# Performance work log

Measured on AMD Instinct MI355X. Metric: run time of the kernel, lower is better.

The kernel has to match this reference:

```python
import jax, jax.numpy as jnp
import numpy as np

HEADS = 2

def gat_layer(x, edge_index, W, att, bias):
    # x: [N, Fin], W: [H*C, Fin], att: [1, H, 2C], bias: [C]
    N = x.shape[0]
    C = bias.shape[0]
    # add self loops (source_to_target: x_j from row 0, aggregate onto row 1)
    loop = jnp.arange(N, dtype=edge_index.dtype)
    src = jnp.concatenate([edge_index[0], loop])
    dst = jnp.concatenate([edge_index[1], loop])
    h = (x @ W.T).reshape(N, HEADS, C)          # [N, H, C]
    x_j = h[src]                                 # [E, H, C]
    x_i = h[dst]                                 # [E, H, C]
    x_cat = jnp.concatenate([x_i, x_j], axis=-1) # [E, H, 2C]
    alpha = (x_cat * att).sum(-1)                # [E, H]
    alpha = jnp.where(alpha >= 0, alpha, 0.2 * alpha)  # leaky_relu(0.2)
    # NOTE: module uses a global (not per-destination) normalization
    alpha = jnp.exp(alpha - alpha.max())
    alpha = alpha / (alpha.sum(axis=0, keepdims=True) + 1e-10)
    msg = x_j * alpha[..., None]                 # [E, H, C]
    aggr = jax.ops.segment_sum(msg, dst, num_segments=N)  # [N, H, C]
    return aggr.mean(axis=1) + bias              # [N, C]

def setup_inputs() -> dict:
    key = jax.random.key(0)
    ks = jax.random.split(key, 7)
    N, Fin, C = 50000, 128, 64
    E = 800000
    x = jax.random.normal(ks[0], (N, Fin), dtype=jnp.float32)
    edge_index = jax.random.randint(ks[1], (2, E), 0, N, dtype=jnp.int64)
    W1 = jax.random.normal(ks[2], (HEADS * C, Fin), dtype=jnp.float32) * 0.05
    att1 = jax.random.normal(ks[3], (1, HEADS, 2 * C), dtype=jnp.float32) * 0.05
    b1 = jnp.zeros((C,), dtype=jnp.float32)
    W2 = jax.random.normal(ks[4], (HEADS * C, C), dtype=jnp.float32) * 0.05
    att2 = jax.random.normal(ks[5], (1, HEADS, 2 * C), dtype=jnp.float32) * 0.05
    b2 = jnp.zeros((C,), dtype=jnp.float32)
    return {"x": x, "edge_index": edge_index, "W1": W1, "att1": att1,
            "b1": b1, "W2": W2, "att2": att2, "b2": b2}

def reference(x, edge_index, W1, att1, b1, W2, att2, b2):
    h = gat_layer(x, edge_index, W1, att1, b1)
    h = jax.nn.relu(h)
    # F.dropout with training flag: treated as eval (identity) for determinism
    out = gat_layer(h, edge_index, W2, att2, b2)
    return out
```

## Files before the change

kernel.cpp:

```cpp
#include <hip/hip_runtime.h>
#include <hip/hip_bf16.h>
#include <math.h>


#define HP 8
#define HG 64
#define NHISTB (HP * HG)
#define HRANGE_MAX 6272
#define NZ    256

using short8 = __attribute__((ext_vector_type(8))) short;
using f32x4  = __attribute__((ext_vector_type(4))) float;

__device__ __forceinline__ unsigned f2bf(float x) {
  unsigned u = __float_as_uint(x);
  return (u + 0x7fffu + ((u >> 16) & 1u)) >> 16;
}
__device__ __forceinline__ float bflo(unsigned p) { return __uint_as_float(p << 16); }
__device__ __forceinline__ float bfhi(unsigned p) { return __uint_as_float(p & 0xffff0000u); }

__global__ __launch_bounds__(256) void init_ws(
    const float* __restrict__ W1, const float* __restrict__ W2,
    unsigned short* __restrict__ wbf1, unsigned short* __restrict__ wbf2,
    float* __restrict__ Z) {
  int tid = blockIdx.x * 256 + threadIdx.x;
  int stride = gridDim.x * 256;
  for (int i = tid; i < 128 * 128; i += stride)
    wbf1[i] = (unsigned short)f2bf(W1[i]);
  for (int i = tid; i < 128 * 64; i += stride)
    wbf2[i] = (unsigned short)f2bf(W2[i]);
  if (tid < 4) Z[tid] = 0.f;
}

template <int FIN>
__global__ __launch_bounds__(256) void gemm_mfma(
    const float* __restrict__ x, const unsigned short* __restrict__ Wb,
    const float* __restrict__ att, unsigned* __restrict__ hq,
    float* __restrict__ si, float* __restrict__ sj,
    int N,
    const int* __restrict__ dstE, int* __restrict__ partial,
    int E, int nhistb, int hstep) {
  const int tid = threadIdx.x;

  constexpr int WB = 128 * FIN * 2;
  constexpr int SMEM = (WB > HRANGE_MAX * 4) ? WB : HRANGE_MAX * 4;
  __shared__ __align__(16) unsigned char smem[SMEM];

  if ((int)blockIdx.x < nhistb) {
    int* lhist = (int*)smem;
    const int p = blockIdx.x & (HP - 1);
    const int g = blockIdx.x >> 3;
    const int lo = p * hstep;
    for (int i = tid; i < hstep; i += 256) lhist[i] = 0;
    __syncthreads();
    const int stride = HG * 256;
    int e = g * 256 + tid;
    for (; e + 3 * stride < E; e += 4 * stride) {
      int d0 = dstE[e] - lo;
      int d1 = dstE[e + stride] - lo;
      int d2 = dstE[e + 2 * stride] - lo;
      int d3 = dstE[e + 3 * stride] - lo;
      if ((unsigned)d0 < (unsigned)hstep) atomicAdd(&lhist[d0], 1);
      if ((unsigned)d1 < (unsigned)hstep) atomicAdd(&lhist[d1], 1);
      if ((unsigned)d2 < (unsigned)hstep) atomicAdd(&lhist[d2], 1);
      if ((unsigned)d3 < (unsigned)hstep) atomicAdd(&lhist[d3], 1);
    }
    for (; e < E; e += stride) {
      int d = dstE[e] - lo;
      if ((unsigned)d < (unsigned)hstep) atomicAdd(&lhist[d], 1);
    }
    __syncthreads();
    for (int i = tid; i < hstep; i += 256) {
      int node = lo + i;
      if (node < N) partial[(size_t)g * N + node] = lhist[i];
    }
    return;
  }

  constexpr int KS = FIN / 32;
  constexpr int CPR = FIN / 8;
  constexpr int NCHUNK = 128 * CPR;

  unsigned short* wlds = (unsigned short*)smem;

  const int w    = tid >> 6;
  const int lane = tid & 63;
  const int cl   = lane & 15;
  const int grp  = lane >> 4;
  const int n0   = (blockIdx.x - nhistb) * 64;

  const int arow = n0 + w * 16 + cl;
  const bool avalid = arow < N;
  float4 av0[KS], av1[KS];
#pragma unroll
  for (int ks = 0; ks < KS; ++ks) {
    av0[ks] = make_float4(0.f, 0.f, 0.f, 0.f);
    av1[ks] = av0[ks];
    if (avalid) {
      const float4* xp =
          (const float4*)(x + (size_t)arow * FIN + ks * 32 + grp * 8);
      av0[ks] = xp[0];
      av1[ks] = xp[1];
    }
  }

  const uint4* Wb4 = (const uint4*)Wb;
  for (int c = tid; c < NCHUNK; c += 256) {
    int row = c / CPR;
    int cc  = c & (CPR - 1);
    *(uint4*)&wlds[row * FIN + ((cc ^ (row & (CPR - 1))) * 8)] = Wb4[c];
  }
  __syncthreads();

  short8 afrag[KS];
#pragma unroll
  for (int ks = 0; ks < KS; ++ks) {
    union { short8 s8; unsigned u[4]; } af;
    af.u[0] = f2bf(av0[ks].x) | (f2bf(av0[ks].y) << 16);
    af.u[1] = f2bf(av0[ks].z) | (f2bf(av0[ks].w) << 16);
    af.u[2] = f2bf(av1[ks].x) | (f2bf(av1[ks].y) << 16);
    af.u[3] = f2bf(av1[ks].z) | (f2bf(av1[ks].w) << 16);
    afrag[ks] = af.s8;
  }

  f32x4 acc[8];
#pragma unroll
  for (int ct = 0; ct < 8; ++ct) acc[ct] = (f32x4){0.f, 0.f, 0.f, 0.f};

  const int swz = cl & (CPR - 1);
#pragma unroll
  for (int ks = 0; ks < KS; ++ks) {
#pragma unroll
    for (int ct = 0; ct < 8; ++ct) {
      const unsigned short* bp =
          &wlds[(ct * 16 + cl) * FIN + (((ks * 4 + grp) ^ swz) * 8)];
      short8 bfrag = *(const short8*)bp;
      acc[ct] = __builtin_amdgcn_mfma_f32_16x16x32_bf16(afrag[ks], bfrag,
                                                        acc[ct], 0, 0, 0);
    }
  }

  float ai[8], aj[8];
#pragma unroll
  for (int ct = 0; ct < 8; ++ct) {
    int hd = ct >> 2;
    int cw = (ct & 3) * 16 + cl;
    ai[ct] = att[hd * 128 + cw];
    aj[ct] = att[hd * 128 + 64 + cw];
  }

#pragma unroll
  for (int r = 0; r < 4; ++r) {
    int node = n0 + w * 16 + grp * 4 + r;
    float s0i = 0.f, s0j = 0.f, s1i = 0.f, s1j = 0.f;
    unsigned wpk[4];
#pragma unroll
    for (int ct = 0; ct < 4; ++ct) {
      float v0 = acc[ct][r];
      float v1 = acc[ct + 4][r];
      s0i += v0 * ai[ct];
      s0j += v0 * aj[ct];
      s1i += v1 * ai[ct + 4];
      s1j += v1 * aj[ct + 4];
      wpk[ct] = f2bf(v0) | (f2bf(v1) << 16);
    }
#pragma unroll
    for (int off = 8; off; off >>= 1) {
      s0i += __shfl_xor(s0i, off, 64);
      s0j += __shfl_xor(s0j, off, 64);
      s1i += __shfl_xor(s1i, off, 64);
      s1j += __shfl_xor(s1j, off, 64);
    }
    if (node < N) {
#pragma unroll
      for (int ct = 0; ct < 4; ++ct)
        hq[(size_t)node * 64 + ct * 16 + cl] = wpk[ct];
      if (cl == 0) {
        si[node * 2 + 0] = s0i;
        si[node * 2 + 1] = s1i;
        sj[node * 2 + 0] = s0j;
        sj[node * 2 + 1] = s1j;
      }
    }
  }
}

__global__ __launch_bounds__(256) void reduce_deg(
    const int* __restrict__ partial, int* __restrict__ deg, int N) {
  int i = blockIdx.x * 256 + threadIdx.x;
  int stride = gridDim.x * 256;
  for (; i < N; i += stride) {
    int s = 0;
#pragma unroll
    for (int g = 0; g < HG; ++g) s += partial[(size_t)g * N + i];
    deg[i] = s;
  }
}

__device__ __forceinline__ void z_edge_body(
    const int* __restrict__ srcE, const int* __restrict__ dstE,
    const float2* __restrict__ si2, const float2* __restrict__ sj2,
    float* __restrict__ Zp, int E, int Etot, int tid0, int stride) {
  float z0 = 0.f, z1 = 0.f;
  for (int e = tid0; e < Etot; e += stride) {
    int s, d;
    if (e < E) { s = srcE[e]; d = dstE[e]; } else { s = d = e - E; }
    float2 siv = si2[d];
    float2 sjv = sj2[s];
    float a0 = siv.x + sjv.x;
    float a1 = siv.y + sjv.y;
    a0 = a0 >= 0.f ? a0 : 0.2f * a0;
    a1 = a1 >= 0.f ? a1 : 0.2f * a1;
    z0 += __expf(a0); z1 += __expf(a1);
  }
  __shared__ float r0[4], r1[4];
  int lane = threadIdx.x & 63, w = threadIdx.x >> 6;
#pragma unroll
  for (int off = 32; off; off >>= 1) {
    z0 += __shfl_down(z0, off, 64);
    z1 += __shfl_down(z1, off, 64);
  }
  if (lane == 0) { r0[w] = z0; r1[w] = z1; }
  __syncthreads();
  if (threadIdx.x == 0) {
    atomicAdd(&Zp[0], r0[0] + r0[1] + r0[2] + r0[3]);
    atomicAdd(&Zp[1], r1[0] + r1[1] + r1[2] + r1[3]);
  }
}

__global__ __launch_bounds__(256) void z_edge(
    const int* __restrict__ srcE, const int* __restrict__ dstE,
    const float2* __restrict__ si2, const float2* __restrict__ sj2,
    float* __restrict__ Zp, int E, int Etot) {
  z_edge_body(srcE, dstE, si2, sj2, Zp, E, Etot,
              blockIdx.x * 256 + threadIdx.x, gridDim.x * 256);
}

__global__ __launch_bounds__(256) void scan_blocks(
    const int* __restrict__ deg, int* __restrict__ rowptr,
    int* __restrict__ bsum, int N) {
  __shared__ int ts[256];
  int b = blockIdx.x, t = threadIdx.x;
  int base = b * 1024 + t * 4;
  int v[4];
#pragma unroll
  for (int j = 0; j < 4; ++j) v[j] = (base + j < N) ? deg[base + j] : 0;
  int tot = v[0] + v[1] + v[2] + v[3];
  ts[t] = tot;
  __syncthreads();
#pragma unroll
  for (int off = 1; off < 256; off <<= 1) {
    int x = (t >= off) ? ts[t - off] : 0;
    __syncthreads();
    ts[t] += x;
    __syncthreads();
  }
  int run = ts[t] - tot;
#pragma unroll
  for (int j = 0; j < 4; ++j) {
    if (base + j < N) rowptr[base + j] = run;
    run += v[j];
  }
  if (t == 255) bsum[b] = ts[255];
}

__global__ __launch_bounds__(256) void scan_finish(
    int* __restrict__ rowptr, const int* __restrict__ bsum,
    int* __restrict__ partial, int N, int Eall, int nb) {
  __shared__ int pre[256];
  if (threadIdx.x == 0) {
    int run = 0;
    for (int i = 0; i < nb; ++i) { pre[i] = run; run += bsum[i]; }
  }
  __syncthreads();
  int tid = blockIdx.x * blockDim.x + threadIdx.x;
  int stride = gridDim.x * blockDim.x;
  for (int i = tid; i < N; i += stride) {
    int v = rowptr[i] + pre[i >> 10];
    rowptr[i] = v;
    int run = v;
#pragma unroll 8
    for (int g = 0; g < HG; ++g) {
      int c = partial[(size_t)g * N + i];
      partial[(size_t)g * N + i] = run;
      run += c;
    }
  }
  if (tid == 0) rowptr[N] = Eall;
}

__global__ __launch_bounds__(256) void scatter_z(
    const int* __restrict__ srcE, const int* __restrict__ dstE,
    const int* __restrict__ partial, int* __restrict__ esrc,
    const float2* __restrict__ si2, const float2* __restrict__ sj2,
    float* __restrict__ Zp, int E, int Etot, int hstep, int N) {
  __shared__ __align__(16) int lcur[HRANGE_MAX];
  if ((int)blockIdx.x < NZ) {
    z_edge_body(srcE, dstE, si2, sj2, Zp, E, Etot,
                blockIdx.x * 256 + threadIdx.x, NZ * 256);
    return;
  }
  const int bid = blockIdx.x - NZ;
  const int p = bid & (HP - 1);
  const int g = bid >> 3;
  const int lo = p * hstep;
  const int tid = threadIdx.x;
  for (int i = tid; i < hstep; i += 256) {
    int node = lo + i;
    lcur[i] = (node < N) ? partial[(size_t)g * N + node] : 0;
  }
  __syncthreads();
  const int stride = HG * 256;
  int e = g * 256 + tid;
  for (; e + 3 * stride < E; e += 4 * stride) {
    int d0 = dstE[e] - lo;
    int d1 = dstE[e + stride] - lo;
    int d2 = dstE[e + 2 * stride] - lo;
    int d3 = dstE[e + 3 * stride] - lo;
    if ((unsigned)d0 < (unsigned)hstep) esrc[atomicAdd(&lcur[d0], 1)] = srcE[e];
    if ((unsigned)d1 < (unsigned)hstep) esrc[atomicAdd(&lcur[d1], 1)] = srcE[e + stride];
    if ((unsigned)d2 < (unsigned)hstep) esrc[atomicAdd(&lcur[d2], 1)] = srcE[e + 2 * stride];
    if ((unsigned)d3 < (unsigned)hstep) esrc[atomicAdd(&lcur[d3], 1)] = srcE[e + 3 * stride];
  }
  for (; e < E; e += stride) {
    int d = dstE[e] - lo;
    if ((unsigned)d < (unsigned)hstep) esrc[atomicAdd(&lcur[d], 1)] = srcE[e];
  }
}

__global__ __launch_bounds__(256) void csr_aggregate(
    const int* __restrict__ rowptr, const int* __restrict__ esrc,
    const unsigned* __restrict__ hq, const float2* __restrict__ si2,
    const float2* __restrict__ sj2, const float* __restrict__ Zp,
    const float* __restrict__ bias, float* __restrict__ out,
    int N, int do_relu) {
  int lane = threadIdx.x & 63;
  int wid = (blockIdx.x * blockDim.x + threadIdx.x) >> 6;
  int nw = (gridDim.x * blockDim.x) >> 6;
  float z0 = 1.f / (Zp[0] + 1e-10f);
  float z1 = 1.f / (Zp[1] + 1e-10f);
  float bv = bias[lane];
  for (int n0 = wid; n0 < N; n0 += nw) {
    int n = __builtin_amdgcn_readfirstlane(n0);
    int beg = rowptr[n], end = rowptr[n + 1];
    float2 siv = si2[n];
    float acc0, acc1;
    {
      float2 jv = sj2[n];
      unsigned p = hq[(size_t)n * 64 + lane];
      float a0 = siv.x + jv.x, a1 = siv.y + jv.y;
      a0 = a0 >= 0.f ? a0 : 0.2f * a0;
      a1 = a1 >= 0.f ? a1 : 0.2f * a1;
      acc0 = bflo(p) * __expf(a0);
      acc1 = bfhi(p) * __expf(a1);
    }
    int k = beg;
    for (; k + 4 <= end; k += 4) {
      int s0 = esrc[k], s1 = esrc[k + 1], s2 = esrc[k + 2], s3 = esrc[k + 3];
      float2 j0 = sj2[s0], j1 = sj2[s1], j2 = sj2[s2], j3 = sj2[s3];
      unsigned p0 = hq[(size_t)s0 * 64 + lane];
      unsigned p1 = hq[(size_t)s1 * 64 + lane];
      unsigned p2 = hq[(size_t)s2 * 64 + lane];
      unsigned p3 = hq[(size_t)s3 * 64 + lane];
      float a00 = siv.x + j0.x, a01 = siv.y + j0.y;
      float a10 = siv.x + j1.x, a11 = siv.y + j1.y;
      float a20 = siv.x + j2.x, a21 = siv.y + j2.y;
      float a30 = siv.x + j3.x, a31 = siv.y + j3.y;
      a00 = a00 >= 0.f ? a00 : 0.2f * a00;  a01 = a01 >= 0.f ? a01 : 0.2f * a01;
      a10 = a10 >= 0.f ? a10 : 0.2f * a10;  a11 = a11 >= 0.f ? a11 : 0.2f * a11;
      a20 = a20 >= 0.f ? a20 : 0.2f * a20;  a21 = a21 >= 0.f ? a21 : 0.2f * a21;
      a30 = a30 >= 0.f ? a30 : 0.2f * a30;  a31 = a31 >= 0.f ? a31 : 0.2f * a31;
      float w00 = __expf(a00), w01 = __expf(a01);
      float w10 = __expf(a10), w11 = __expf(a11);
      float w20 = __expf(a20), w21 = __expf(a21);
      float w30 = __expf(a30), w31 = __expf(a31);
      acc0 += bflo(p0) * w00 + bflo(p1) * w10 + bflo(p2) * w20 + bflo(p3) * w30;
      acc1 += bfhi(p0) * w01 + bfhi(p1) * w11 + bfhi(p2) * w21 + bfhi(p3) * w31;
    }
    for (; k < end; ++k) {
      int s = esrc[k];
      float2 jv = sj2[s];
      unsigned p = hq[(size_t)s * 64 + lane];
      float a0 = siv.x + jv.x, a1 = siv.y + jv.y;
      a0 = a0 >= 0.f ? a0 : 0.2f * a0;
      a1 = a1 >= 0.f ? a1 : 0.2f * a1;
      acc0 += bflo(p) * __expf(a0);
      acc1 += bfhi(p) * __expf(a1);
    }
    float r = 0.5f * (acc0 * z0 + acc1 * z1) + bv;
    if (do_relu) r = fmaxf(r, 0.f);
    out[(size_t)n * 64 + lane] = r;
  }
}

extern "C" void kernel_launch(void* const* d_in, const int* in_sizes, int n_in,
                              void* d_out, int out_size, void* d_ws, size_t ws_size,
                              hipStream_t stream) {
  const float* x    = (const float*)d_in[0];
  const int*   ei   = (const int*)d_in[1];
  const float* W1   = (const float*)d_in[2];
  const float* att1 = (const float*)d_in[3];
  const float* b1   = (const float*)d_in[4];
  const float* W2   = (const float*)d_in[5];
  const float* att2 = (const float*)d_in[6];
  const float* b2   = (const float*)d_in[7];
  float* out = (float*)d_out;

  const int N = in_sizes[0] / 128;
  const int E = in_sizes[1] / 2;
  const int Etot = E + N;
  const int* srcE = ei;
  const int* dstE = ei + E;

  unsigned* hq = (unsigned*)d_ws;
  float* si    = (float*)(hq + (size_t)N * 64);
  float* sj    = si + (size_t)N * 2;
  float* Z     = sj + (size_t)N * 2;
  float* x2    = Z + 4;
  int* partial = (int*)x2;
  int* rowptr  = (int*)(x2 + (size_t)N * 64);
  int* deg     = rowptr + (N + 1);
  int* esrc    = deg + N;
  int* bsum    = esrc + E;
  uintptr_t wp = ((uintptr_t)(bsum + 256) + 15) & ~(uintptr_t)15;
  unsigned short* wbf1 = (unsigned short*)wp;
  unsigned short* wbf2 = wbf1 + 128 * 128;

  dim3 blk(256);
  int nb = (N + 1023) / 1024;
  int ntiles = (N + 63) / 64;
  int hstep = (N + HP - 1) / HP;

  init_ws<<<64, blk, 0, stream>>>(W1, W2, wbf1, wbf2, Z);
  gemm_mfma<128><<<NHISTB + ntiles, blk, 0, stream>>>(
      x, wbf1, att1, hq, si, sj, N, dstE, partial, E, NHISTB, hstep);
  reduce_deg<<<256, blk, 0, stream>>>(partial, deg, N);
  scan_blocks<<<nb, blk, 0, stream>>>(deg, rowptr, bsum, N);
  scan_finish<<<256, blk, 0, stream>>>(rowptr, bsum, partial, N, E, nb);
  scatter_z<<<NZ + NHISTB, blk, 0, stream>>>(
      srcE, dstE, partial, esrc, (const float2*)si, (const float2*)sj,
      Z, E, Etot, hstep, N);
  csr_aggregate<<<4096, blk, 0, stream>>>(rowptr, esrc, hq, (const float2*)si,
                                          (const float2*)sj, Z, b1, x2, N, 1);
  gemm_mfma<64><<<ntiles, blk, 0, stream>>>(
      x2, wbf2, att2, hq, si, sj, N, dstE, partial, E, 0, hstep);
  z_edge<<<NZ, blk, 0, stream>>>(srcE, dstE, (const float2*)si,
                                 (const float2*)sj, Z + 2, E, Etot);
  csr_aggregate<<<4096, blk, 0, stream>>>(rowptr, esrc, hq, (const float2*)si,
                                          (const float2*)sj, Z + 2, b2, out, N, 0);
}
```

Baseline: 261.5 us.

## Interleave two destination nodes per wave in CSR aggregation and fuse degree reduction into scan

The CSR aggregation kernel now processes two destination nodes per wavefront, interleaving their 4-edge gather batches so more independent loads are in flight. The grid is halved to match. Separately, the reduce_deg kernel is removed and scan_blocks sums the per-group histogram partials directly with int4 loads, dropping one launch and the deg buffer. Risks are higher register pressure and imbalance when the two nodes have very different degrees.

Result: slower. 277.9 us (+6.3%).

```diff
diff --git a/kernel.cpp b/kernel.cpp
--- a/kernel.cpp
+++ b/kernel.cpp
@@ -18,6 +18,10 @@
 }
 __device__ __forceinline__ float bflo(unsigned p) { return __uint_as_float(p << 16); }
 __device__ __forceinline__ float bfhi(unsigned p) { return __uint_as_float(p & 0xffff0000u); }
+__device__ __forceinline__ float lrexp(float a) {
+  a = a >= 0.f ? a : 0.2f * a;
+  return __expf(a);
+}
 
 __global__ __launch_bounds__(256) void init_ws(
     const float* __restrict__ W1, const float* __restrict__ W2,
@@ -185,18 +189,6 @@
   }
 }
 
-__global__ __launch_bounds__(256) void reduce_deg(
-    const int* __restrict__ partial, int* __restrict__ deg, int N) {
-  int i = blockIdx.x * 256 + threadIdx.x;
-  int stride = gridDim.x * 256;
-  for (; i < N; i += stride) {
-    int s = 0;
-#pragma unroll
-    for (int g = 0; g < HG; ++g) s += partial[(size_t)g * N + i];
-    deg[i] = s;
-  }
-}
-
 __device__ __forceinline__ void z_edge_body(
     const int* __restrict__ srcE, const int* __restrict__ dstE,
     const float2* __restrict__ si2, const float2* __restrict__ sj2,
@@ -207,11 +199,8 @@
     if (e < E) { s = srcE[e]; d = dstE[e]; } else { s = d = e - E; }
     float2 siv = si2[d];
     float2 sjv = sj2[s];
-    float a0 = siv.x + sjv.x;
-    float a1 = siv.y + sjv.y;
-    a0 = a0 >= 0.f ? a0 : 0.2f * a0;
-    a1 = a1 >= 0.f ? a1 : 0.2f * a1;
-    z0 += __expf(a0); z1 += __expf(a1);
+    z0 += lrexp(siv.x + sjv.x);
+    z1 += lrexp(siv.y + sjv.y);
   }
   __shared__ float r0[4], r1[4];
   int lane = threadIdx.x & 63, w = threadIdx.x >> 6;
@@ -237,15 +226,22 @@
 }
 
 __global__ __launch_bounds__(256) void scan_blocks(
-    const int* __restrict__ deg, int* __restrict__ rowptr,
+    const int* __restrict__ partial, int* __restrict__ rowptr,
     int* __restrict__ bsum, int N) {
   __shared__ int ts[256];
   int b = blockIdx.x, t = threadIdx.x;
   int base = b * 1024 + t * 4;
-  int v[4];
-#pragma unroll
-  for (int j = 0; j < 4; ++j) v[j] = (base + j < N) ? deg[base + j] : 0;
-  int tot = v[0] + v[1] + v[2] + v[3];
+  int s0 = 0, s1 = 0, s2 = 0, s3 = 0;
+  if (base < N) {
+    const int4* p4 = (const int4*)partial;
+#pragma unroll 4
+    for (int g = 0; g < HG; ++g) {
+      int4 v = p4[((size_t)g * N + base) >> 2];
+      s0 += v.x; s1 += v.y; s2 += v.z; s3 += v.w;
+    }
+  }
+  int v[4] = {s0, s1, s2, s3};
+  int tot = s0 + s1 + s2 + s3;
   ts[t] = tot;
   __syncthreads();
 #pragma unroll
@@ -328,6 +324,30 @@
   }
 }
 
+__device__ __forceinline__ void edge4(
+    const int* __restrict__ esrc, int k, const float2* __restrict__ sj2,
+    const unsigned* __restrict__ hq, int lane, float2 siv,
+    float& acc0, float& acc1) {
+  int s0 = esrc[k], s1 = esrc[k + 1], s2 = esrc[k + 2], s3 = esrc[k + 3];
+  float2 j0 = sj2[s0], j1 = sj2[s1], j2 = sj2[s2], j3 = sj2[s3];
+  unsigned p0 = hq[(size_t)s0 * 64 + lane];
+  unsigned p1 = hq[(size_t)s1 * 64 + lane];
+  unsigned p2 = hq[(size_t)s2 * 64 + lane];
+  unsigned p3 = hq[(size_t)s3 * 64 + lane];
+  acc0 += bflo(p0) * lrexp(siv.x + j0.x) + bflo(p1) * lrexp(siv.x + j1.x) +
+          bflo(p2) * lrexp(siv.x + j2.x) + bflo(p3) * lrexp(siv.x + j3.x);
+  acc1 += bfhi(p0) * lrexp(siv.y + j0.y) + bfhi(p1) * lrexp(siv.y + j1.y) +
+          bfhi(p2) * lrexp(siv.y + j2.y) + bfhi(p3) * lrexp(siv.y + j3.y);
+}
+__device__ __forceinline__ void edge1(
+    int s, const float2* __restrict__ sj2, const unsigned* __restrict__ hq,
+    int lane, float2 siv, float& acc0, float& acc1) {
+  float2 jv = sj2[s];
+  unsigned p = hq[(size_t)s * 64 + lane];
+  acc0 += bflo(p) * lrexp(siv.x + jv.x);
+  acc1 += bfhi(p) * lrexp(siv.y + jv.y);
+}
+
 __global__ __launch_bounds__(256) void csr_aggregate(
     const int* __restrict__ rowptr, const int* __restrict__ esrc,
     const unsigned* __restrict__ hq, const float2* __restrict__ si2,
@@ -340,56 +360,46 @@
   float z0 = 1.f / (Zp[0] + 1e-10f);
   float z1 = 1.f / (Zp[1] + 1e-10f);
   float bv = bias[lane];
-  for (int n0 = wid; n0 < N; n0 += nw) {
-    int n = __builtin_amdgcn_readfirstlane(n0);
-    int beg = rowptr[n], end = rowptr[n + 1];
-    float2 siv = si2[n];
-    float acc0, acc1;
-    {
-      float2 jv = sj2[n];
-      unsigned p = hq[(size_t)n * 64 + lane];
-      float a0 = siv.x + jv.x, a1 = siv.y + jv.y;
-      a0 = a0 >= 0.f ? a0 : 0.2f * a0;
-      a1 = a1 >= 0.f ? a1 : 0.2f * a1;
-      acc0 = bflo(p) * __expf(a0);
-      acc1 = bfhi(p) * __expf(a1);
-    }
-    int k = beg;
-    for (; k + 4 <= end; k += 4) {
-      int s0 = esrc[k], s1 = esrc[k + 1], s2 = esrc[k + 2], s3 = esrc[k + 3];
-      float2 j0 = sj2[s0], j1 = sj2[s1], j2 = sj2[s2], j3 = sj2[s3];
-      unsigned p0 = hq[(size_t)s0 * 64 + lane];
-      unsigned p1 = hq[(size_t)s1 * 64 + lane];
-      unsigned p2 = hq[(size_t)s2 * 64 + lane];
-      unsigned p3 = hq[(size_t)s3 * 64 + lane];
-      float a00 = siv.x + j0.x, a01 = siv.y + j0.y;
-      float a10 = siv.x + j1.x, a11 = siv.y + j1.y;
-      float a20 = siv.x + j2.x, a21 = siv.y + j2.y;
-      float a30 = siv.x + j3.x, a31 = siv.y + j3.y;
-      a00 = a00 >= 0.f ? a00 : 0.2f * a00;  a01 = a01 >= 0.f ? a01 : 0.2f * a01;
-      a10 = a10 >= 0.f ? a10 : 0.2f * a10;  a11 = a11 >= 0.f ? a11 : 0.2f * a11;
-      a20 = a20 >= 0.f ? a20 : 0.2f * a20;  a21 = a21 >= 0.f ? a21 : 0.2f * a21;
-      a30 = a30 >= 0.f ? a30 : 0.2f * a30;  a31 = a31 >= 0.f ? a31 : 0.2f * a31;
-      float w00 = __expf(a00), w01 = __expf(a01);
-      float w10 = __expf(a10), w11 = __expf(a11);
-      float w20 = __expf(a20), w21 = __expf(a21);
-      float w30 = __expf(a30), w31 = __expf(a31);
-      acc0 += bflo(p0) * w00 + bflo(p1) * w10 + bflo(p2) * w20 + bflo(p3) * w30;
-      acc1 += bfhi(p0) * w01 + bfhi(p1) * w11 + bfhi(p2) * w21 + bfhi(p3) * w31;
-    }
-    for (; k < end; ++k) {
-      int s = esrc[k];
-      float2 jv = sj2[s];
-      unsigned p = hq[(size_t)s * 64 + lane];
-      float a0 = siv.x + jv.x, a1 = siv.y + jv.y;
-      a0 = a0 >= 0.f ? a0 : 0.2f * a0;
-      a1 = a1 >= 0.f ? a1 : 0.2f * a1;
-      acc0 += bflo(p) * __expf(a0);
-      acc1 += bfhi(p) * __expf(a1);
-    }
-    float r = 0.5f * (acc0 * z0 + acc1 * z1) + bv;
-    if (do_relu) r = fmaxf(r, 0.f);
-    out[(size_t)n * 64 + lane] = r;
+  for (int n0 = wid; n0 < N; n0 += 2 * nw) {
+    const int na = __builtin_amdgcn_readfirstlane(n0);
+    const bool hasB = (n0 + nw) < N;
+    const int nbv = __builtin_amdgcn_readfirstlane(hasB ? n0 + nw : n0);
+
+    int begA = rowptr[na], endA = rowptr[na + 1];
+    float2 sivA = si2[na];
+    float accA0 = 0.f, accA1 = 0.f;
+    edge1(na, sj2, hq, lane, sivA, accA0, accA1);
+
+    int begB = 0, endB = 0;
+    float2 sivB = make_float2(0.f, 0.f);
+    float accB0 = 0.f, accB1 = 0.f;
+    if (hasB) {
+      begB = rowptr[nbv];
+      endB = rowptr[nbv + 1];
+      sivB = si2[nbv];
+      edge1(nbv, sj2, hq, lane, sivB, accB0, accB1);
+    }
+
+    int ka = begA, kb = begB;
+    while (ka + 4 <= endA && kb + 4 <= endB) {
+      edge4(esrc, ka, sj2, hq, lane, sivA, accA0, accA1);
+      edge4(esrc, kb, sj2, hq, lane, sivB, accB0, accB1);
+      ka += 4;
+      kb += 4;
+    }
+    for (; ka + 4 <= endA; ka += 4) edge4(esrc, ka, sj2, hq, lane, sivA, accA0, accA1);
+    for (; ka < endA; ++ka) edge1(esrc[ka], sj2, hq, lane, sivA, accA0, accA1);
+    for (; kb + 4 <= endB; kb += 4) edge4(esrc, kb, sj2, hq, lane, sivB, accB0, accB1);
+    for (; kb < endB; ++kb) edge1(esrc[kb], sj2, hq, lane, sivB, accB0, accB1);
+
+    float rA = 0.5f * (accA0 * z0 + accA1 * z1) + bv;
+    if (do_relu) rA = fmaxf(rA, 0.f);
+    out[(size_t)na * 64 + lane] = rA;
+    if (hasB) {
+      float rB = 0.5f * (accB0 * z0 + accB1 * z1) + bv;
+      if (do_relu) rB = fmaxf(rB, 0.f);
+      out[(size_t)nbv * 64 + lane] = rB;
+    }
   }
 }
 
@@ -419,8 +429,7 @@
   float* x2    = Z + 4;
   int* partial = (int*)x2;
   int* rowptr  = (int*)(x2 + (size_t)N * 64);
-  int* deg     = rowptr + (N + 1);
-  int* esrc    = deg + N;
+  int* esrc    = rowptr + (N + 1);
   int* bsum    = esrc + E;
   uintptr_t wp = ((uintptr_t)(bsum + 256) + 15) & ~(uintptr_t)15;
   unsigned short* wbf1 = (unsigned short*)wp;
@@ -434,18 +443,17 @@
   init_ws<<<64, blk, 0, stream>>>(W1, W2, wbf1, wbf2, Z);
   gemm_mfma<128><<<NHISTB + ntiles, blk, 0, stream>>>(
       x, wbf1, att1, hq, si, sj, N, dstE, partial, E, NHISTB, hstep);
-  reduce_deg<<<256, blk, 0, stream>>>(partial, deg, N);
-  scan_blocks<<<nb, blk, 0, stream>>>(deg, rowptr, bsum, N);
+  scan_blocks<<<nb, blk, 0, stream>>>(partial, rowptr, bsum, N);
   scan_finish<<<256, blk, 0, stream>>>(rowptr, bsum, partial, N, E, nb);
   scatter_z<<<NZ + NHISTB, blk, 0, stream>>>(
       srcE, dstE, partial, esrc, (const float2*)si, (const float2*)sj,
       Z, E, Etot, hstep, N);
-  csr_aggregate<<<4096, blk, 0, stream>>>(rowptr, esrc, hq, (const float2*)si,
+  csr_aggregate<<<2048, blk, 0, stream>>>(rowptr, esrc, hq, (const float2*)si,
                                           (const float2*)sj, Z, b1, x2, N, 1);
   gemm_mfma<64><<<ntiles, blk, 0, stream>>>(
       x2, wbf2, att2, hq, si, sj, N, dstE, partial, E, 0, hstep);
   z_edge<<<NZ, blk, 0, stream>>>(srcE, dstE, (const float2*)si,
                                  (const float2*)sj, Z + 2, E, Etot);
-  csr_aggregate<<<4096, blk, 0, stream>>>(rowptr, esrc, hq, (const float2*)si,
+  csr_aggregate<<<2048, blk, 0, stream>>>(rowptr, esrc, hq, (const float2*)si,
                                           (const float2*)sj, Z + 2, b2, out, N, 0);
 }
```
